# Kernel tuning notes

Hardware: AMD Instinct MI355X
Metric: run time of the kernel (lower is better)

The kernel has to match this reference:

```python
import jax, jax.numpy as jnp
import numpy as np

N = 8192        # num_nodes
F = 512         # num_features
H1 = 32         # FLAGS.hidden1
H2 = 16         # FLAGS.hidden2
E = 131072      # nnz of normalized adjacency
SAMPLING_NUM = 1000  # averaging 1000 N(0,1) draws == one N(0, 1/1000) draw


def setup_inputs() -> dict:
    key = jax.random.key(0)
    ks = jax.random.split(key, 10)
    inv_sqrt_s = 1.0 / np.sqrt(SAMPLING_NUM)
    return {
        "features": jax.random.normal(ks[0], (N, F), dtype=jnp.float32),
        "adj_rows": jax.random.randint(ks[1], (E,), 0, N, dtype=jnp.int32),
        "adj_cols": jax.random.randint(ks[2], (E,), 0, N, dtype=jnp.int32),
        "adj_val": jax.random.uniform(ks[3], (E,), dtype=jnp.float32),
        "W0": jax.random.normal(ks[4], (F, H1), dtype=jnp.float32) * 0.1,
        "W1": jax.random.normal(ks[5], (H1, H2), dtype=jnp.float32) * 0.1,
        "W2": jax.random.normal(ks[6], (H1, H2), dtype=jnp.float32) * 0.1,
        "W3": jax.random.normal(ks[7], (H1, H2), dtype=jnp.float32) * 0.1,
        # averaged MC samples: mean of 1000 N(0,1) draws ~ N(0, 1/1000)
        "sample_1": jax.random.normal(ks[8], (N, H2), dtype=jnp.float32) * inv_sqrt_s,
        "sample_2": jax.random.normal(ks[9], (N, H2), dtype=jnp.float32) * inv_sqrt_s,
    }


def _spmm(rows, cols, vals, x):
    # sparse (N x N) @ dense (N x d) via gather + segment-sum
    gathered = vals[:, None] * x[cols]          # [E, d]
    return jax.ops.segment_sum(gathered, rows, num_segments=N)


def reference(features, adj_rows, adj_cols, adj_val, W0, W1, W2, W3, sample_1, sample_2):
    # GraphConvolutionSparse: relu(A @ (X W0))  (dropout disabled / inference)
    h1 = jax.nn.relu(_spmm(adj_rows, adj_cols, adj_val, features @ W0))   # [N, H1]
    # Three GraphConvolution heads
    z_ex = _spmm(adj_rows, adj_cols, adj_val, h1 @ W1)                    # identity act
    z_log_en = jax.nn.softmax(_spmm(adj_rows, adj_cols, adj_val, h1 @ W2), axis=-1)
    z_log_he = jax.nn.softmax(_spmm(adj_rows, adj_cols, adj_val, h1 @ W3), axis=-1)
    z_en = jnp.exp(z_log_en)
    z_he = 0.1 * jnp.exp(z_log_he)
    # double reparameterization with averaged MC samples
    z_enn = z_en + sample_1 * z_he
    z = z_ex + sample_2 * z_enn                                           # [N, H2]
    # InnerProductDecoder: flatten(z z^T)
    return (z @ z.T).reshape(-1)                                          # [N*N]
```

## Files before the change

kernel.cpp:

```cpp
#include <hip/hip_runtime.h>
#include <math.h>

#define N_NODES 8192
#define F_IN    512
#define H1      32
#define H2      16

#define FMA4(acc, s, v) do { (acc).x += (s)*(v).x; (acc).y += (s)*(v).y; \
                             (acc).z += (s)*(v).z; (acc).w += (s)*(v).w; } while(0)

__global__ __launch_bounds__(256) void k_xw0(const float* __restrict__ feat,
                                             const float* __restrict__ W0,
                                             float* __restrict__ xw0) {
    __shared__ float w0s[F_IN * H1];
    float4* w0s_v = (float4*)w0s;
    const float4* W0_v = (const float4*)W0;
    int t = threadIdx.x;
    #pragma unroll
    for (int i = 0; i < 16; ++i) w0s_v[t + i * 256] = W0_v[t + i * 256];
    __syncthreads();

    int row = blockIdx.x * 32 + (t >> 3);
    int cg  = (t & 7) * 4;
    const float4* frow_v = (const float4*)(feat + (size_t)row * F_IN);

    float4 acc = {0.f, 0.f, 0.f, 0.f};
    #pragma unroll 4
    for (int k0 = 0; k0 < F_IN; k0 += 4) {
        float4 f  = frow_v[k0 >> 2];
        float4 w0 = *(float4*)&w0s[(k0 + 0) * H1 + cg];
        float4 w1 = *(float4*)&w0s[(k0 + 1) * H1 + cg];
        float4 w2 = *(float4*)&w0s[(k0 + 2) * H1 + cg];
        float4 w3 = *(float4*)&w0s[(k0 + 3) * H1 + cg];
        FMA4(acc, f.x, w0);
        FMA4(acc, f.y, w1);
        FMA4(acc, f.z, w2);
        FMA4(acc, f.w, w3);
    }
    *(float4*)&xw0[row * H1 + cg] = acc;
}

__global__ __launch_bounds__(256) void k_hist(const int* __restrict__ rows,
                                              int* __restrict__ cnt, int E) {
    int e = blockIdx.x * 256 + threadIdx.x;
    if (e < E) atomicAdd(&cnt[rows[e]], 1);
}

__global__ __launch_bounds__(256) void k_scan(const int* __restrict__ cnt,
                                              int* __restrict__ row_start,
                                              int* __restrict__ cursor) {
    __shared__ int part[256];
    int t = threadIdx.x;
    int base = t * 32;
    int local[32];
    int s = 0;
    #pragma unroll
    for (int i = 0; i < 32; ++i) { local[i] = cnt[base + i]; s += local[i]; }
    part[t] = s;
    __syncthreads();
    for (int off = 1; off < 256; off <<= 1) {
        int v = (t >= off) ? part[t - off] : 0;
        __syncthreads();
        part[t] += v;
        __syncthreads();
    }
    int run = (t == 0) ? 0 : part[t - 1];
    #pragma unroll
    for (int i = 0; i < 32; ++i) {
        row_start[base + i] = run;
        cursor[base + i]    = run;
        run += local[i];
    }
    if (t == 255) row_start[N_NODES] = run;
}

__global__ __launch_bounds__(256) void k_scatter(const int* __restrict__ rows,
                                                 const int* __restrict__ cols,
                                                 const float* __restrict__ vals,
                                                 int* __restrict__ cursor,
                                                 int2* __restrict__ edges, int E) {
    int e = blockIdx.x * 256 + threadIdx.x;
    if (e >= E) return;
    int pos = atomicAdd(&cursor[rows[e]], 1);
    edges[pos] = make_int2(cols[e], __float_as_int(vals[e]));
}

__global__ __launch_bounds__(256) void k_spmm1(const int* __restrict__ row_start,
                                               const int2* __restrict__ edges,
                                               const float* __restrict__ xw0,
                                               float* __restrict__ h1) {
    int t  = blockIdx.x * 256 + threadIdx.x;
    int r  = t >> 4;
    int tt = t & 15;
    int part = (tt & 7) * 4;
    int half = tt >> 3;
    int s = row_start[r], e = row_start[r + 1];
    float4 acc = {0.f, 0.f, 0.f, 0.f};
    for (int i = s + half; i < e; i += 2) {
        int2 ed = edges[i];
        float v = __int_as_float(ed.y);
        float4 x = *(const float4*)&xw0[ed.x * H1 + part];
        FMA4(acc, v, x);
    }
    acc.x += __shfl_xor(acc.x, 8);
    acc.y += __shfl_xor(acc.y, 8);
    acc.z += __shfl_xor(acc.z, 8);
    acc.w += __shfl_xor(acc.w, 8);
    if (half == 0) {
        acc.x = fmaxf(acc.x, 0.f); acc.y = fmaxf(acc.y, 0.f);
        acc.z = fmaxf(acc.z, 0.f); acc.w = fmaxf(acc.w, 0.f);
        *(float4*)&h1[r * H1 + part] = acc;
    }
}

__global__ __launch_bounds__(256) void k_heads(const float* __restrict__ h1,
                                               const float* __restrict__ W1,
                                               const float* __restrict__ W2,
                                               const float* __restrict__ W3,
                                               float* __restrict__ Y) {
    __shared__ float ws[3 * H1 * H2];
    int t = threadIdx.x;
    for (int i = t; i < H1 * H2; i += 256) {
        ws[i]        = W1[i];
        ws[512 + i]  = W2[i];
        ws[1024 + i] = W3[i];
    }
    __syncthreads();

    int g   = blockIdx.x * 256 + t;
    int row = g >> 4, col = g & 15;
    const float* h = &h1[row * H1];
    float a0 = 0.f, a1 = 0.f, a2 = 0.f;
    #pragma unroll
    for (int k = 0; k < H1; ++k) {
        float hv = h[k];
        a0 += hv * ws[k * H2 + col];
        a1 += hv * ws[512 + k * H2 + col];
        a2 += hv * ws[1024 + k * H2 + col];
    }
    float* yr = &Y[row * 48];
    yr[col]      = a0;
    yr[16 + col] = a1;
    yr[32 + col] = a2;
}

__global__ __launch_bounds__(256) void k_spmm3(const int* __restrict__ row_start,
                                               const int2* __restrict__ edges,
                                               const float* __restrict__ Y,
                                               float* __restrict__ T) {
    int t  = blockIdx.x * 256 + threadIdx.x;
    int r  = t >> 4;
    int tt = t & 15;
    int cg = (tt & 3) * 4;
    int q  = tt >> 2;
    int s = row_start[r], e = row_start[r + 1];
    float4 a0 = {0,0,0,0}, a1 = {0,0,0,0}, a2 = {0,0,0,0};
    for (int i = s + q; i < e; i += 4) {
        int2 ed = edges[i];
        float v = __int_as_float(ed.y);
        const float* y = &Y[ed.x * 48];
        float4 y0 = *(const float4*)&y[cg];
        float4 y1 = *(const float4*)&y[16 + cg];
        float4 y2 = *(const float4*)&y[32 + cg];
        FMA4(a0, v, y0);
        FMA4(a1, v, y1);
        FMA4(a2, v, y2);
    }
#define RED4(a) do { \
        (a).x += __shfl_xor((a).x, 4); (a).y += __shfl_xor((a).y, 4); \
        (a).z += __shfl_xor((a).z, 4); (a).w += __shfl_xor((a).w, 4); \
        (a).x += __shfl_xor((a).x, 8); (a).y += __shfl_xor((a).y, 8); \
        (a).z += __shfl_xor((a).z, 8); (a).w += __shfl_xor((a).w, 8); } while(0)
    RED4(a0); RED4(a1); RED4(a2);
    if (q == 0) {
        float* tr = &T[r * 48];
        *(float4*)&tr[cg]      = a0;
        *(float4*)&tr[16 + cg] = a1;
        *(float4*)&tr[32 + cg] = a2;
    }
}

__global__ __launch_bounds__(256) void k_final(const float* __restrict__ T,
                                               const float* __restrict__ s1,
                                               const float* __restrict__ s2,
                                               float* __restrict__ z) {
    int r = blockIdx.x * 256 + threadIdx.x;
    if (r >= N_NODES) return;
    const float* tex = T + r * 48;
    const float* ten = tex + 16;
    const float* the = tex + 32;

    float en[H2], he[H2];
    float m1 = -1e30f, m2 = -1e30f;
    #pragma unroll
    for (int k = 0; k < H2; ++k) {
        en[k] = ten[k];
        he[k] = the[k];
        m1 = fmaxf(m1, en[k]);
        m2 = fmaxf(m2, he[k]);
    }
    float sum1 = 0.f, sum2 = 0.f;
    #pragma unroll
    for (int k = 0; k < H2; ++k) {
        en[k] = expf(en[k] - m1);  sum1 += en[k];
        he[k] = expf(he[k] - m2);  sum2 += he[k];
    }
    float inv1 = 1.f / sum1, inv2 = 1.f / sum2;
    #pragma unroll
    for (int k = 0; k < H2; ++k) {
        float z_en = expf(en[k] * inv1);
        float z_he = 0.1f * expf(he[k] * inv2);
        float z_enn = z_en + s1[r * H2 + k] * z_he;
        z[r * H2 + k] = tex[k] + s2[r * H2 + k] * z_enn;
    }
}

__global__ __launch_bounds__(256) void k_zzt(const float* __restrict__ z,
                                             float* __restrict__ out) {
    __shared__ float zi[64 * 17];
    __shared__ float zjT[H2 * 64];
    int t  = threadIdx.x;
    int i0 = blockIdx.y * 64, j0 = blockIdx.x * 64;

    {
        int c = t >> 2, q = (t & 3) * 4;
        float4 a = *(const float4*)&z[(i0 + c) * H2 + q];
        zi[c * 17 + q + 0] = a.x; zi[c * 17 + q + 1] = a.y;
        zi[c * 17 + q + 2] = a.z; zi[c * 17 + q + 3] = a.w;
        float4 b = *(const float4*)&z[(j0 + c) * H2 + q];
        zjT[(q + 0) * 64 + c] = b.x; zjT[(q + 1) * 64 + c] = b.y;
        zjT[(q + 2) * 64 + c] = b.z; zjT[(q + 3) * 64 + c] = b.w;
    }
    __syncthreads();

    int tx = t & 15, ty = t >> 4;
    float4 acc0 = {0,0,0,0}, acc1 = {0,0,0,0}, acc2 = {0,0,0,0}, acc3 = {0,0,0,0};
    const float4* zjT_v = (const float4*)zjT;
    #pragma unroll
    for (int k = 0; k < H2; ++k) {
        float4 b  = zjT_v[k * 16 + tx];
        float  a0 = zi[(ty * 4 + 0) * 17 + k];
        float  a1 = zi[(ty * 4 + 1) * 17 + k];
        float  a2 = zi[(ty * 4 + 2) * 17 + k];
        float  a3 = zi[(ty * 4 + 3) * 17 + k];
        FMA4(acc0, a0, b);
        FMA4(acc1, a1, b);
        FMA4(acc2, a2, b);
        FMA4(acc3, a3, b);
    }
    size_t base = (size_t)(i0 + ty * 4) * N_NODES + j0 + tx * 4;
    *(float4*)&out[base]               = acc0;
    *(float4*)&out[base + N_NODES]     = acc1;
    *(float4*)&out[base + 2 * N_NODES] = acc2;
    *(float4*)&out[base + 3 * N_NODES] = acc3;
}

extern "C" void kernel_launch(void* const* d_in, const int* in_sizes, int n_in,
                              void* d_out, int out_size, void* d_ws, size_t ws_size,
                              hipStream_t stream) {
    const float* feat = (const float*)d_in[0];
    const int*   rows = (const int*)d_in[1];
    const int*   cols = (const int*)d_in[2];
    const float* vals = (const float*)d_in[3];
    const float* W0   = (const float*)d_in[4];
    const float* W1   = (const float*)d_in[5];
    const float* W2   = (const float*)d_in[6];
    const float* W3   = (const float*)d_in[7];
    const float* s1   = (const float*)d_in[8];
    const float* s2   = (const float*)d_in[9];
    float* out = (float*)d_out;
    int E = in_sizes[1];

    float* ws        = (float*)d_ws;
    float* xw0       = ws;
    float* h1        = ws + 262144;
    float* Y         = ws + 524288;
    float* T         = ws + 917504;
    float* z         = ws + 1310720;
    int*   cnt       = (int*)(ws + 1441792);
    int*   row_start = (int*)(ws + 1449984);
    int*   cursor    = (int*)(ws + 1458432);
    int2*  edges     = (int2*)(ws + 1466624);

    hipMemsetAsync(cnt, 0, N_NODES * sizeof(int), stream);

    k_hist   <<<(E + 255) / 256, 256, 0, stream>>>(rows, cnt, E);
    k_scan   <<<1, 256, 0, stream>>>(cnt, row_start, cursor);
    k_scatter<<<(E + 255) / 256, 256, 0, stream>>>(rows, cols, vals, cursor, edges, E);

    k_xw0  <<<N_NODES / 32, 256, 0, stream>>>(feat, W0, xw0);
    k_spmm1<<<N_NODES * 16 / 256, 256, 0, stream>>>(row_start, edges, xw0, h1);
    k_heads<<<N_NODES * H2 / 256, 256, 0, stream>>>(h1, W1, W2, W3, Y);
    k_spmm3<<<N_NODES * 16 / 256, 256, 0, stream>>>(row_start, edges, Y, T);
    k_final<<<N_NODES / 256, 256, 0, stream>>>(T, s1, s2, z);

    dim3 grid(N_NODES / 64, N_NODES / 64);
    k_zzt<<<grid, 256, 0, stream>>>(z, out);
}
```

Baseline: 359.2 us.

## Fuse SpMM stages with head projection and softmax epilogue, drop memset

Merges the first SpMM with the three head projections (via intra-group shuffles), and the second SpMM with the softmax/reparameterization epilogue, removing the h1 and T intermediates and two launches. The cnt zeroing moves into the X·W0 kernel, which now launches first, replacing the memset. The scan now stages counts through padded shared memory so its global reads are coalesced. Total runtime is likely dominated by the 256 MB z·zᵀ output write, so these savings on small pre-stages are minor.

```diff
diff --git a/kernel.cpp b/kernel.cpp
--- a/kernel.cpp
+++ b/kernel.cpp
@@ -9,13 +9,23 @@
 #define FMA4(acc, s, v) do { (acc).x += (s)*(v).x; (acc).y += (s)*(v).y; \
                              (acc).z += (s)*(v).z; (acc).w += (s)*(v).w; } while(0)
 
+#define RED4(a) do { \
+        (a).x += __shfl_xor((a).x, 4); (a).y += __shfl_xor((a).y, 4); \
+        (a).z += __shfl_xor((a).z, 4); (a).w += __shfl_xor((a).w, 4); \
+        (a).x += __shfl_xor((a).x, 8); (a).y += __shfl_xor((a).y, 8); \
+        (a).z += __shfl_xor((a).z, 8); (a).w += __shfl_xor((a).w, 8); } while(0)
+
 __global__ __launch_bounds__(256) void k_xw0(const float* __restrict__ feat,
                                              const float* __restrict__ W0,
-                                             float* __restrict__ xw0) {
+                                             float* __restrict__ xw0,
+                                             int* __restrict__ cnt) {
+    int t = threadIdx.x;
+    int gid = blockIdx.x * 256 + t;
+    if (gid < N_NODES) cnt[gid] = 0;
+
     __shared__ float w0s[F_IN * H1];
     float4* w0s_v = (float4*)w0s;
     const float4* W0_v = (const float4*)W0;
-    int t = threadIdx.x;
     #pragma unroll
     for (int i = 0; i < 16; ++i) w0s_v[t + i * 256] = W0_v[t + i * 256];
     __syncthreads();
@@ -49,13 +59,20 @@
 __global__ __launch_bounds__(256) void k_scan(const int* __restrict__ cnt,
                                               int* __restrict__ row_start,
                                               int* __restrict__ cursor) {
+    __shared__ int buf[N_NODES + 256];
     __shared__ int part[256];
     int t = threadIdx.x;
+    #pragma unroll
+    for (int i = 0; i < 32; ++i) {
+        int v = t + i * 256;
+        buf[v + (v >> 5)] = cnt[v];
+    }
+    __syncthreads();
     int base = t * 32;
     int local[32];
     int s = 0;
     #pragma unroll
-    for (int i = 0; i < 32; ++i) { local[i] = cnt[base + i]; s += local[i]; }
+    for (int i = 0; i < 32; ++i) { local[i] = buf[33 * t + i]; s += local[i]; }
     part[t] = s;
     __syncthreads();
     for (int off = 1; off < 256; off <<= 1) {
@@ -85,12 +102,24 @@
     edges[pos] = make_int2(cols[e], __float_as_int(vals[e]));
 }
 
-__global__ __launch_bounds__(256) void k_spmm1(const int* __restrict__ row_start,
-                                               const int2* __restrict__ edges,
-                                               const float* __restrict__ xw0,
-                                               float* __restrict__ h1) {
-    int t  = blockIdx.x * 256 + threadIdx.x;
-    int r  = t >> 4;
+__global__ __launch_bounds__(256) void k_spmm1h(const int* __restrict__ row_start,
+                                                const int2* __restrict__ edges,
+                                                const float* __restrict__ xw0,
+                                                const float* __restrict__ W1,
+                                                const float* __restrict__ W2,
+                                                const float* __restrict__ W3,
+                                                float* __restrict__ Y) {
+    __shared__ float ws[3 * H1 * H2];
+    int t = threadIdx.x;
+    for (int i = t; i < H1 * H2; i += 256) {
+        ws[i]        = W1[i];
+        ws[512 + i]  = W2[i];
+        ws[1024 + i] = W3[i];
+    }
+    __syncthreads();
+
+    int g  = blockIdx.x * 256 + t;
+    int r  = g >> 4;
     int tt = t & 15;
     int part = (tt & 7) * 4;
     int half = tt >> 3;
@@ -106,48 +135,36 @@
     acc.y += __shfl_xor(acc.y, 8);
     acc.z += __shfl_xor(acc.z, 8);
     acc.w += __shfl_xor(acc.w, 8);
-    if (half == 0) {
-        acc.x = fmaxf(acc.x, 0.f); acc.y = fmaxf(acc.y, 0.f);
-        acc.z = fmaxf(acc.z, 0.f); acc.w = fmaxf(acc.w, 0.f);
-        *(float4*)&h1[r * H1 + part] = acc;
-    }
-}
-
-__global__ __launch_bounds__(256) void k_heads(const float* __restrict__ h1,
-                                               const float* __restrict__ W1,
-                                               const float* __restrict__ W2,
-                                               const float* __restrict__ W3,
-                                               float* __restrict__ Y) {
-    __shared__ float ws[3 * H1 * H2];
-    int t = threadIdx.x;
-    for (int i = t; i < H1 * H2; i += 256) {
-        ws[i]        = W1[i];
-        ws[512 + i]  = W2[i];
-        ws[1024 + i] = W3[i];
-    }
-    __syncthreads();
-
-    int g   = blockIdx.x * 256 + t;
-    int row = g >> 4, col = g & 15;
-    const float* h = &h1[row * H1];
+    acc.x = fmaxf(acc.x, 0.f); acc.y = fmaxf(acc.y, 0.f);
+    acc.z = fmaxf(acc.z, 0.f); acc.w = fmaxf(acc.w, 0.f);
+
     float a0 = 0.f, a1 = 0.f, a2 = 0.f;
     #pragma unroll
-    for (int k = 0; k < H1; ++k) {
-        float hv = h[k];
-        a0 += hv * ws[k * H2 + col];
-        a1 += hv * ws[512 + k * H2 + col];
-        a2 += hv * ws[1024 + k * H2 + col];
-    }
-    float* yr = &Y[row * 48];
-    yr[col]      = a0;
-    yr[16 + col] = a1;
-    yr[32 + col] = a2;
-}
-
-__global__ __launch_bounds__(256) void k_spmm3(const int* __restrict__ row_start,
-                                               const int2* __restrict__ edges,
-                                               const float* __restrict__ Y,
-                                               float* __restrict__ T) {
+    for (int sI = 0; sI < 8; ++sI) {
+        float hx = __shfl(acc.x, sI, 16);
+        float hy = __shfl(acc.y, sI, 16);
+        float hz = __shfl(acc.z, sI, 16);
+        float hw = __shfl(acc.w, sI, 16);
+        int k = sI * 4;
+        a0 += hx * ws[(k+0)*16 + tt]        + hy * ws[(k+1)*16 + tt]
+            + hz * ws[(k+2)*16 + tt]        + hw * ws[(k+3)*16 + tt];
+        a1 += hx * ws[512 + (k+0)*16 + tt]  + hy * ws[512 + (k+1)*16 + tt]
+            + hz * ws[512 + (k+2)*16 + tt]  + hw * ws[512 + (k+3)*16 + tt];
+        a2 += hx * ws[1024 + (k+0)*16 + tt] + hy * ws[1024 + (k+1)*16 + tt]
+            + hz * ws[1024 + (k+2)*16 + tt] + hw * ws[1024 + (k+3)*16 + tt];
+    }
+    float* yr = &Y[r * 48];
+    yr[tt]      = a0;
+    yr[16 + tt] = a1;
+    yr[32 + tt] = a2;
+}
+
+__global__ __launch_bounds__(256) void k_spmm3f(const int* __restrict__ row_start,
+                                                const int2* __restrict__ edges,
+                                                const float* __restrict__ Y,
+                                                const float* __restrict__ s1,
+                                                const float* __restrict__ s2,
+                                                float* __restrict__ z) {
     int t  = blockIdx.x * 256 + threadIdx.x;
     int r  = t >> 4;
     int tt = t & 15;
@@ -159,60 +176,38 @@
         int2 ed = edges[i];
         float v = __int_as_float(ed.y);
         const float* y = &Y[ed.x * 48];
-        float4 y0 = *(const float4*)&y[cg];
-        float4 y1 = *(const float4*)&y[16 + cg];
-        float4 y2 = *(const float4*)&y[32 + cg];
-        FMA4(a0, v, y0);
-        FMA4(a1, v, y1);
-        FMA4(a2, v, y2);
-    }
-#define RED4(a) do { \
-        (a).x += __shfl_xor((a).x, 4); (a).y += __shfl_xor((a).y, 4); \
-        (a).z += __shfl_xor((a).z, 4); (a).w += __shfl_xor((a).w, 4); \
-        (a).x += __shfl_xor((a).x, 8); (a).y += __shfl_xor((a).y, 8); \
-        (a).z += __shfl_xor((a).z, 8); (a).w += __shfl_xor((a).w, 8); } while(0)
+        FMA4(a0, v, *(const float4*)&y[cg]);
+        FMA4(a1, v, *(const float4*)&y[16 + cg]);
+        FMA4(a2, v, *(const float4*)&y[32 + cg]);
+    }
     RED4(a0); RED4(a1); RED4(a2);
-    if (q == 0) {
-        float* tr = &T[r * 48];
-        *(float4*)&tr[cg]      = a0;
-        *(float4*)&tr[16 + cg] = a1;
-        *(float4*)&tr[32 + cg] = a2;
-    }
-}
-
-__global__ __launch_bounds__(256) void k_final(const float* __restrict__ T,
-                                               const float* __restrict__ s1,
-                                               const float* __restrict__ s2,
-                                               float* __restrict__ z) {
-    int r = blockIdx.x * 256 + threadIdx.x;
-    if (r >= N_NODES) return;
-    const float* tex = T + r * 48;
-    const float* ten = tex + 16;
-    const float* the = tex + 32;
-
-    float en[H2], he[H2];
-    float m1 = -1e30f, m2 = -1e30f;
-    #pragma unroll
-    for (int k = 0; k < H2; ++k) {
-        en[k] = ten[k];
-        he[k] = the[k];
-        m1 = fmaxf(m1, en[k]);
-        m2 = fmaxf(m2, he[k]);
-    }
-    float sum1 = 0.f, sum2 = 0.f;
-    #pragma unroll
-    for (int k = 0; k < H2; ++k) {
-        en[k] = expf(en[k] - m1);  sum1 += en[k];
-        he[k] = expf(he[k] - m2);  sum2 += he[k];
-    }
+
+    float m1 = fmaxf(fmaxf(a1.x, a1.y), fmaxf(a1.z, a1.w));
+    m1 = fmaxf(m1, __shfl_xor(m1, 1));
+    m1 = fmaxf(m1, __shfl_xor(m1, 2));
+    float m2 = fmaxf(fmaxf(a2.x, a2.y), fmaxf(a2.z, a2.w));
+    m2 = fmaxf(m2, __shfl_xor(m2, 1));
+    m2 = fmaxf(m2, __shfl_xor(m2, 2));
+
+    float4 e1, e2;
+    e1.x = expf(a1.x - m1); e1.y = expf(a1.y - m1);
+    e1.z = expf(a1.z - m1); e1.w = expf(a1.w - m1);
+    e2.x = expf(a2.x - m2); e2.y = expf(a2.y - m2);
+    e2.z = expf(a2.z - m2); e2.w = expf(a2.w - m2);
+    float sum1 = e1.x + e1.y + e1.z + e1.w;
+    sum1 += __shfl_xor(sum1, 1); sum1 += __shfl_xor(sum1, 2);
+    float sum2 = e2.x + e2.y + e2.z + e2.w;
+    sum2 += __shfl_xor(sum2, 1); sum2 += __shfl_xor(sum2, 2);
     float inv1 = 1.f / sum1, inv2 = 1.f / sum2;
-    #pragma unroll
-    for (int k = 0; k < H2; ++k) {
-        float z_en = expf(en[k] * inv1);
-        float z_he = 0.1f * expf(he[k] * inv2);
-        float z_enn = z_en + s1[r * H2 + k] * z_he;
-        z[r * H2 + k] = tex[k] + s2[r * H2 + k] * z_enn;
-    }
+
+    float4 sv1 = *(const float4*)&s1[r * H2 + cg];
+    float4 sv2 = *(const float4*)&s2[r * H2 + cg];
+    float4 zr;
+    zr.x = a0.x + sv2.x * (expf(e1.x * inv1) + sv1.x * 0.1f * expf(e2.x * inv2));
+    zr.y = a0.y + sv2.y * (expf(e1.y * inv1) + sv1.y * 0.1f * expf(e2.y * inv2));
+    zr.z = a0.z + sv2.z * (expf(e1.z * inv1) + sv1.z * 0.1f * expf(e2.z * inv2));
+    zr.w = a0.w + sv2.w * (expf(e1.w * inv1) + sv1.w * 0.1f * expf(e2.w * inv2));
+    if (q == 0) *(float4*)&z[r * H2 + cg] = zr;
 }
 
 __global__ __launch_bounds__(256) void k_zzt(const float* __restrict__ z,
@@ -223,13 +218,13 @@
     int i0 = blockIdx.y * 64, j0 = blockIdx.x * 64;
 
     {
-        int c = t >> 2, q = (t & 3) * 4;
-        float4 a = *(const float4*)&z[(i0 + c) * H2 + q];
-        zi[c * 17 + q + 0] = a.x; zi[c * 17 + q + 1] = a.y;
-        zi[c * 17 + q + 2] = a.z; zi[c * 17 + q + 3] = a.w;
-        float4 b = *(const float4*)&z[(j0 + c) * H2 + q];
-        zjT[(q + 0) * 64 + c] = b.x; zjT[(q + 1) * 64 + c] = b.y;
-        zjT[(q + 2) * 64 + c] = b.z; zjT[(q + 3) * 64 + c] = b.w;
+        int c = t >> 2, qq = (t & 3) * 4;
+        float4 a = *(const float4*)&z[(i0 + c) * H2 + qq];
+        zi[c * 17 + qq + 0] = a.x; zi[c * 17 + qq + 1] = a.y;
+        zi[c * 17 + qq + 2] = a.z; zi[c * 17 + qq + 3] = a.w;
+        float4 b = *(const float4*)&z[(j0 + c) * H2 + qq];
+        zjT[(qq + 0) * 64 + c] = b.x; zjT[(qq + 1) * 64 + c] = b.y;
+        zjT[(qq + 2) * 64 + c] = b.z; zjT[(qq + 3) * 64 + c] = b.w;
     }
     __syncthreads();
 
@@ -273,26 +268,19 @@
 
     float* ws        = (float*)d_ws;
     float* xw0       = ws;
-    float* h1        = ws + 262144;
-    float* Y         = ws + 524288;
-    float* T         = ws + 917504;
-    float* z         = ws + 1310720;
-    int*   cnt       = (int*)(ws + 1441792);
-    int*   row_start = (int*)(ws + 1449984);
-    int*   cursor    = (int*)(ws + 1458432);
-    int2*  edges     = (int2*)(ws + 1466624);
-
-    hipMemsetAsync(cnt, 0, N_NODES * sizeof(int), stream);
-
+    float* Y         = ws + 262144;
+    float* z         = ws + 655360;
+    int*   cnt       = (int*)(ws + 786432);
+    int*   row_start = (int*)(ws + 794624);
+    int*   cursor    = (int*)(ws + 803072);
+    int2*  edges     = (int2*)(ws + 811264);
+
+    k_xw0    <<<N_NODES / 32, 256, 0, stream>>>(feat, W0, xw0, cnt);
     k_hist   <<<(E + 255) / 256, 256, 0, stream>>>(rows, cnt, E);
     k_scan   <<<1, 256, 0, stream>>>(cnt, row_start, cursor);
     k_scatter<<<(E + 255) / 256, 256, 0, stream>>>(rows, cols, vals, cursor, edges, E);
-
-    k_xw0  <<<N_NODES / 32, 256, 0, stream>>>(feat, W0, xw0);
-    k_spmm1<<<N_NODES * 16 / 256, 256, 0, stream>>>(row_start, edges, xw0, h1);
-    k_heads<<<N_NODES * H2 / 256, 256, 0, stream>>>(h1, W1, W2, W3, Y);
-    k_spmm3<<<N_NODES * 16 / 256, 256, 0, stream>>>(row_start, edges, Y, T);
-    k_final<<<N_NODES / 256, 256, 0, stream>>>(T, s1, s2, z);
+    k_spmm1h <<<N_NODES * 16 / 256, 256, 0, stream>>>(row_start, edges, xw0, W1, W2, W3, Y);
+    k_spmm3f <<<N_NODES * 16 / 256, 256, 0, stream>>>(row_start, edges, Y, s1, s2, z);
 
     dim3 grid(N_NODES / 64, N_NODES / 64);
     k_zzt<<<grid, 256, 0, stream>>>(z, out);
```

Measured after the change: 363.6 us. About the same (+1.2%).
